# Kernel tuning notes

Hardware: AMD Instinct MI355X
Metric: run time of the kernel (lower is better)

## Reference

```python
import jax, jax.numpy as jnp
import numpy as np

D_MODEL = 1024
NUM_HEADS = 16
HEAD_DIM = D_MODEL // NUM_HEADS


def setup_inputs() -> dict:
    key = jax.random.key(0)
    ks = jax.random.split(key, 11)
    B, N = 2, 2048
    s = 1.0 / np.sqrt(D_MODEL)
    return {
        "query": jax.random.normal(ks[0], (B, N, D_MODEL), jnp.float32),
        "key":   jax.random.normal(ks[1], (B, N, D_MODEL), jnp.float32),
        "value": jax.random.normal(ks[2], (B, N, D_MODEL), jnp.float32),
        "Wq": jax.random.normal(ks[3], (D_MODEL, D_MODEL), jnp.float32) * s,
        "bq": jax.random.normal(ks[4], (D_MODEL,), jnp.float32) * 0.01,
        "Wk": jax.random.normal(ks[5], (D_MODEL, D_MODEL), jnp.float32) * s,
        "bk": jax.random.normal(ks[6], (D_MODEL,), jnp.float32) * 0.01,
        "Wv": jax.random.normal(ks[7], (D_MODEL, D_MODEL), jnp.float32) * s,
        "bv": jax.random.normal(ks[8], (D_MODEL,), jnp.float32) * 0.01,
        "Wo": jax.random.normal(ks[9], (D_MODEL, D_MODEL), jnp.float32) * s,
        "bo": jax.random.normal(ks[10], (D_MODEL,), jnp.float32) * 0.01,
    }


def _split_heads(x):
    # [B, N, d_model] -> [B, H, N, head_dim]
    B, N, _ = x.shape
    return x.reshape(B, N, NUM_HEADS, HEAD_DIM).transpose(0, 2, 1, 3)


def reference(query, key, value, Wq, bq, Wk, bk, Wv, bv, Wo, bo):
    B, N, _ = query.shape
    q = _split_heads(query @ Wq.T + bq)  # [B,H,N,dh]
    k = _split_heads(key @ Wk.T + bk)
    v = _split_heads(value @ Wv.T + bv)
    # NOTE: faithful to source: no 1/sqrt(head_dim) scaling.
    scores = jnp.einsum("bhnd,bhmd->bhnm", q, k)
    attn = jax.nn.softmax(scores, axis=-1)
    out = jnp.einsum("bhnm,bhmd->bhnd", attn, v)
    out = out.transpose(0, 2, 1, 3).reshape(B, N, D_MODEL)
    return out @ Wo.T + bo
```

## Files before the change

kernel.cpp:

```cpp
#include <hip/hip_runtime.h>
#include <cstdint>

#define DEV __device__ __forceinline__

typedef __bf16 bf16x8 __attribute__((ext_vector_type(8)));
typedef short s16x8 __attribute__((ext_vector_type(8)));
typedef float f32x4 __attribute__((ext_vector_type(4)));
typedef unsigned short u16;

constexpr int D_MODEL = 1024;
constexpr int SEQ = 2048;
constexpr float LOG2E = 1.4426950408889634f;
constexpr float SHIFT = 64.0f;

DEV u16 f2bf(float f) {
  uint32_t u = __float_as_uint(f);
  u += 0x7fff + ((u >> 16) & 1);
  return (u16)(u >> 16);
}

DEV void load_lds16(const void* g, void* l) {
  __builtin_amdgcn_global_load_lds((const __attribute__((address_space(1))) void*)g,
                                   (__attribute__((address_space(3))) void*)l, 16, 0, 0);
}

struct ConvArgs {
  const float* src[7];
  u16* dst[7];
  int n[7];
};

__global__ __launch_bounds__(256) void convert_kernel(ConvArgs a) {
  const int t = blockIdx.y;
  const int i = (blockIdx.x * 256 + threadIdx.x) * 4;
  if (i >= a.n[t]) return;
  const float4 v = *(const float4*)(a.src[t] + i);
  ushort4 o;
  o.x = f2bf(v.x); o.y = f2bf(v.y); o.z = f2bf(v.z); o.w = f2bf(v.w);
  *(ushort4*)(a.dst[t] + i) = o;
}

struct GemmArgs {
  const u16* A[3];
  const u16* W[3];
  const float* bias[3];
  void* out[3];
  float scale[3];
  int mode;
};

__global__ __launch_bounds__(256) void gemm_nt(GemmArgs args) {
  __shared__ u16 lA[128 * 64];
  __shared__ u16 lB[128 * 64];
  const int z = blockIdx.z;
  const u16* __restrict__ A = args.A[z];
  const u16* __restrict__ W = args.W[z];
  const int tid = threadIdx.x;
  const int lane = tid & 63, wid = tid >> 6;
  const int quad = lane >> 4, l16 = lane & 15;
  const int wm = wid >> 1, wn = wid & 1;
  const int m0 = blockIdx.y * 128;
  const int n0 = blockIdx.x * 128;

  f32x4 acc[4][4] = {};

  for (int kt = 0; kt < D_MODEL / 64; ++kt) {
    const int k0 = kt * 64;
#pragma unroll
    for (int p = 0; p < 4; ++p) {
      int c = p * 256 + tid;
      int row = c >> 3;
      int g = ((c & 7) ^ (row & 7)) * 8;
      load_lds16(A + (size_t)(m0 + row) * D_MODEL + k0 + g, &lA[c * 8]);
      load_lds16(W + (size_t)(n0 + row) * D_MODEL + k0 + g, &lB[c * 8]);
    }
    __syncthreads();
#pragma unroll
    for (int ks = 0; ks < 2; ++ks) {
      bf16x8 af[4], bfr[4];
#pragma unroll
      for (int mt = 0; mt < 4; ++mt) {
        int r = wm * 64 + mt * 16 + l16;
        int ch = (ks * 4 + quad) ^ (r & 7);
        af[mt] = *(const bf16x8*)&lA[r * 64 + ch * 8];
      }
#pragma unroll
      for (int nt = 0; nt < 4; ++nt) {
        int r = wn * 64 + nt * 16 + l16;
        int ch = (ks * 4 + quad) ^ (r & 7);
        bfr[nt] = *(const bf16x8*)&lB[r * 64 + ch * 8];
      }
#pragma unroll
      for (int mt = 0; mt < 4; ++mt)
#pragma unroll
        for (int nt = 0; nt < 4; ++nt)
          acc[mt][nt] = __builtin_amdgcn_mfma_f32_16x16x32_bf16(af[mt], bfr[nt], acc[mt][nt], 0, 0, 0);
    }
    __syncthreads();
  }

  const float* __restrict__ bias = args.bias[z];
  if (args.mode == 0) {
    u16* out = (u16*)args.out[z];
    float sc = args.scale[z];
#pragma unroll
    for (int nt = 0; nt < 4; ++nt) {
      int col = n0 + wn * 64 + nt * 16 + l16;
      float bv = bias[col];
      int h = col >> 6, d = col & 63;
#pragma unroll
      for (int mt = 0; mt < 4; ++mt) {
        int mb = m0 + wm * 64 + mt * 16 + quad * 4;
#pragma unroll
        for (int r = 0; r < 4; ++r) {
          int tok = mb + r;
          int b = tok >> 11, tt = tok & 2047;
          out[(((size_t)(b * 16 + h) * SEQ + tt) << 6) + d] = f2bf((acc[mt][nt][r] + bv) * sc);
        }
      }
    }
  } else {
    float* out = (float*)args.out[z];
#pragma unroll
    for (int nt = 0; nt < 4; ++nt) {
      int col = n0 + wn * 64 + nt * 16 + l16;
      float bv = bias[col];
#pragma unroll
      for (int mt = 0; mt < 4; ++mt) {
        int mb = m0 + wm * 64 + mt * 16 + quad * 4;
#pragma unroll
        for (int r = 0; r < 4; ++r)
          out[(size_t)(mb + r) * D_MODEL + col] = acc[mt][nt][r] + bv;
      }
    }
  }
}

__global__ __launch_bounds__(256) void transpose_v(const u16* __restrict__ V, u16* __restrict__ Vt) {
  __shared__ u16 tile[64][66];
  const int bh = blockIdx.y;
  const int t0 = blockIdx.x * 64;
  const int tid = threadIdx.x;
  const u16* src = V + ((size_t)bh * SEQ + t0) * 64;
#pragma unroll
  for (int p = 0; p < 4; ++p) {
    int v = p * 256 + tid;
    int row = v >> 4, c4 = (v & 15) * 4;
    ushort4 x = *(const ushort4*)(src + (size_t)row * 64 + c4);
    tile[row][c4] = x.x; tile[row][c4 + 1] = x.y; tile[row][c4 + 2] = x.z; tile[row][c4 + 3] = x.w;
  }
  __syncthreads();
  u16* dst = Vt + (size_t)bh * 64 * SEQ + t0;
#pragma unroll
  for (int p = 0; p < 4; ++p) {
    int v = p * 256 + tid;
    int d = v >> 4, c4 = (v & 15) * 4;
    ushort4 o;
    o.x = tile[c4][d]; o.y = tile[c4 + 1][d]; o.z = tile[c4 + 2][d]; o.w = tile[c4 + 3][d];
    *(ushort4*)(dst + (size_t)d * SEQ + c4) = o;
  }
}

__global__ __launch_bounds__(128, 2) void attn_kernel(const u16* __restrict__ Q,
                                                      const u16* __restrict__ K,
                                                      const u16* __restrict__ Vt,
                                                      u16* __restrict__ O) {
  __shared__ u16 sm[2][2][64 * 64];
  const int bid = blockIdx.x;
  const int xcd = bid & 7, jj = bid >> 3;
  const int bh = xcd + 8 * (jj >> 5);
  const int q0 = (jj & 31) * 64;
  const int tid = threadIdx.x;
  const int lane = tid & 63, w = tid >> 6;
  const int quad = lane >> 4, l16 = lane & 15;

  const u16* kbase = K + (size_t)bh * SEQ * 64;
  const u16* vtbase = Vt + (size_t)bh * 64 * SEQ;

  bf16x8 qf[4][2];
#pragma unroll
  for (int qh = 0; qh < 4; ++qh) {
    const u16* qrow = Q + ((size_t)bh * SEQ + q0 + qh * 16 + l16) * 64;
    qf[qh][0] = *(const bf16x8*)(qrow + quad * 8);
    qf[qh][1] = *(const bf16x8*)(qrow + 32 + quad * 8);
  }

  bf16x8 onesA;
  {
    __bf16 v = (l16 == 0) ? (__bf16)1.0f : (__bf16)0.0f;
#pragma unroll
    for (int j = 0; j < 8; ++j) onesA[j] = v;
  }

  f32x4 acc[4][5] = {};
  const f32x4 minit = {-SHIFT, -SHIFT, -SHIFT, -SHIFT};

#define STAGE(T, B)                                                               \
  {                                                                               \
    _Pragma("unroll")                                                             \
    for (int p = 0; p < 4; ++p) {                                                 \
      int c = p * 128 + tid;                                                      \
      int row = c >> 3;                                                           \
      int km = (row & 32) | (((row >> 2) & 3) << 3) | (((row >> 4) & 1) << 2) |   \
               (row & 3);                                                         \
      int g = ((c & 7) ^ (row & 7)) * 8;                                          \
      load_lds16(kbase + (size_t)((T) * 64 + km) * 64 + g, &sm[B][0][c * 8]);     \
      load_lds16(vtbase + (size_t)row * SEQ + (T) * 64 + g, &sm[B][1][c * 8]);    \
    }                                                                             \
  }

  STAGE(0, 0);
  __syncthreads();

  for (int t = 0; t < SEQ / 64; ++t) {
    if (t + 1 < SEQ / 64) STAGE(t + 1, (t + 1) & 1);
    const u16* lK = sm[t & 1][0];
    const u16* lV = sm[t & 1][1];

    bf16x8 kf[2][2];
#pragma unroll
    for (int nt = 0; nt < 2; ++nt) {
      int r = w * 32 + nt * 16 + l16;
#pragma unroll
      for (int ks = 0; ks < 2; ++ks) {
        int ch = (ks * 4 + quad) ^ (r & 7);
        kf[nt][ks] = *(const bf16x8*)&lK[r * 64 + ch * 8];
      }
    }

    s16x8 pf[4];
#pragma unroll
    for (int qh = 0; qh < 4; ++qh) {
      f32x4 s0 = __builtin_amdgcn_mfma_f32_16x16x32_bf16(kf[0][0], qf[qh][0], minit, 0, 0, 0);
      s0 = __builtin_amdgcn_mfma_f32_16x16x32_bf16(kf[0][1], qf[qh][1], s0, 0, 0, 0);
      f32x4 s1 = __builtin_amdgcn_mfma_f32_16x16x32_bf16(kf[1][0], qf[qh][0], minit, 0, 0, 0);
      s1 = __builtin_amdgcn_mfma_f32_16x16x32_bf16(kf[1][1], qf[qh][1], s1, 0, 0, 0);
      bf16x8 pb;
#pragma unroll
      for (int r = 0; r < 4; ++r) {
        pb[r] = (__bf16)__builtin_amdgcn_exp2f(s0[r]);
        pb[4 + r] = (__bf16)__builtin_amdgcn_exp2f(s1[r]);
      }
      pf[qh] = __builtin_bit_cast(s16x8, pb);
    }

#pragma unroll
    for (int dt = 0; dt < 4; ++dt) {
      int row = dt * 16 + l16;
      int ch = (w * 4 + quad) ^ (row & 7);
      bf16x8 vf = *(const bf16x8*)&lV[row * 64 + ch * 8];
#pragma unroll
      for (int qh = 0; qh < 4; ++qh)
        acc[qh][dt] = __builtin_amdgcn_mfma_f32_16x16x32_bf16(
            vf, __builtin_bit_cast(bf16x8, pf[qh]), acc[qh][dt], 0, 0, 0);
    }
#pragma unroll
    for (int qh = 0; qh < 4; ++qh)
      acc[qh][4] = __builtin_amdgcn_mfma_f32_16x16x32_bf16(
          onesA, __builtin_bit_cast(bf16x8, pf[qh]), acc[qh][4], 0, 0, 0);

    __syncthreads();
  }
#undef STAGE

  float* red = (float*)&sm[0][0][0];
  if (w == 1) {
#pragma unroll
    for (int qh = 0; qh < 4; ++qh)
#pragma unroll
      for (int dt = 0; dt < 5; ++dt)
        *(f32x4*)&red[((qh * 5 + dt) * 64 + lane) * 4] = acc[qh][dt];
  }
  __syncthreads();
  if (w == 0) {
    const int b = bh >> 4, h = bh & 15;
#pragma unroll
    for (int qh = 0; qh < 4; ++qh) {
#pragma unroll
      for (int dt = 0; dt < 5; ++dt)
        acc[qh][dt] += *(const f32x4*)&red[((qh * 5 + dt) * 64 + lane) * 4];
      float sum = __shfl(acc[qh][4][0], l16, 64);
      float inv = 1.0f / sum;
      const int tok = b * SEQ + q0 + qh * 16 + l16;
      u16* obase = O + (size_t)tok * D_MODEL + h * 64;
#pragma unroll
      for (int dt = 0; dt < 4; ++dt) {
        ushort4 o;
        o.x = f2bf(acc[qh][dt][0] * inv);
        o.y = f2bf(acc[qh][dt][1] * inv);
        o.z = f2bf(acc[qh][dt][2] * inv);
        o.w = f2bf(acc[qh][dt][3] * inv);
        *(ushort4*)(obase + dt * 16 + quad * 4) = o;
      }
    }
  }
}

extern "C" void kernel_launch(void* const* d_in, const int* in_sizes, int n_in,
                              void* d_out, int out_size, void* d_ws, size_t ws_size,
                              hipStream_t stream) {
  const float* q  = (const float*)d_in[0];
  const float* k  = (const float*)d_in[1];
  const float* v  = (const float*)d_in[2];
  const float* Wq = (const float*)d_in[3];
  const float* bq = (const float*)d_in[4];
  const float* Wk = (const float*)d_in[5];
  const float* bk = (const float*)d_in[6];
  const float* Wv = (const float*)d_in[7];
  const float* bv = (const float*)d_in[8];
  const float* Wo = (const float*)d_in[9];
  const float* bo = (const float*)d_in[10];

  uint8_t* ws = (uint8_t*)d_ws;
  const size_t MB = 1024 * 1024;
  u16* Xq  = (u16*)(ws + 0 * MB);
  u16* Xk  = (u16*)(ws + 8 * MB);
  u16* Xv  = (u16*)(ws + 16 * MB);
  u16* Wqb = (u16*)(ws + 24 * MB);
  u16* Wkb = (u16*)(ws + 26 * MB);
  u16* Wvb = (u16*)(ws + 28 * MB);
  u16* Wob = (u16*)(ws + 30 * MB);
  u16* Qb  = (u16*)(ws + 32 * MB);
  u16* Kb  = (u16*)(ws + 40 * MB);
  u16* Vb  = (u16*)(ws + 48 * MB);
  u16* Vtb = Xk;
  u16* Ob  = Xq;

  ConvArgs ca;
  ca.src[0] = q;  ca.dst[0] = Xq;  ca.n[0] = 4194304;
  ca.src[1] = k;  ca.dst[1] = Xk;  ca.n[1] = 4194304;
  ca.src[2] = v;  ca.dst[2] = Xv;  ca.n[2] = 4194304;
  ca.src[3] = Wq; ca.dst[3] = Wqb; ca.n[3] = 1048576;
  ca.src[4] = Wk; ca.dst[4] = Wkb; ca.n[4] = 1048576;
  ca.src[5] = Wv; ca.dst[5] = Wvb; ca.n[5] = 1048576;
  ca.src[6] = Wo; ca.dst[6] = Wob; ca.n[6] = 1048576;
  convert_kernel<<<dim3(4096, 7), 256, 0, stream>>>(ca);

  GemmArgs ga;
  ga.A[0] = Xq; ga.A[1] = Xk; ga.A[2] = Xv;
  ga.W[0] = Wqb; ga.W[1] = Wkb; ga.W[2] = Wvb;
  ga.bias[0] = bq; ga.bias[1] = bk; ga.bias[2] = bv;
  ga.out[0] = Qb; ga.out[1] = Kb; ga.out[2] = Vb;
  ga.scale[0] = LOG2E; ga.scale[1] = 1.0f; ga.scale[2] = 1.0f;
  ga.mode = 0;
  gemm_nt<<<dim3(8, 32, 3), 256, 0, stream>>>(ga);

  transpose_v<<<dim3(32, 32), 256, 0, stream>>>(Vb, Vtb);

  attn_kernel<<<dim3(1024), 128, 0, stream>>>(Qb, Kb, Vtb, Ob);

  GemmArgs g2;
  g2.A[0] = Ob; g2.A[1] = Ob; g2.A[2] = Ob;
  g2.W[0] = Wob; g2.W[1] = Wob; g2.W[2] = Wob;
  g2.bias[0] = bo; g2.bias[1] = bo; g2.bias[2] = bo;
  g2.out[0] = d_out; g2.out[1] = d_out; g2.out[2] = d_out;
  g2.scale[0] = 1.0f; g2.scale[1] = 1.0f; g2.scale[2] = 1.0f;
  g2.mode = 1;
  gemm_nt<<<dim3(8, 32, 1), 256, 0, stream>>>(g2);
}
```

Baseline: 231.2 us.

## Double-buffer GEMM LDS, XCD-aware block mapping, split-K output projection with atomics

The GEMM kernel now double-buffers its LDS tiles so the next K-slice loads while MFMAs run on the current one. Blocks are launched on a 1-D grid and remapped so that each XCD gets contiguous M rows, which should improve L2 reuse. The output projection is split four ways along K and accumulated with float atomicAdd into an output that the convert kernel first fills with the bias. This adds parallelism for the small final GEMM, at the cost of atomic traffic, doubled LDS use and a non-deterministic summation order.

Measured after the change: 256.2 us. +10.8%, slower.

```diff
diff --git a/kernel.cpp b/kernel.cpp
--- a/kernel.cpp
+++ b/kernel.cpp
@@ -25,15 +25,21 @@
 }
 
 struct ConvArgs {
-  const float* src[7];
+  const float* src[8];
   u16* dst[7];
-  int n[7];
+  float* dstf;
+  int n[8];
 };
 
 __global__ __launch_bounds__(256) void convert_kernel(ConvArgs a) {
   const int t = blockIdx.y;
   const int i = (blockIdx.x * 256 + threadIdx.x) * 4;
   if (i >= a.n[t]) return;
+  if (t == 7) {
+    float4 b = *(const float4*)(a.src[7] + (i & 1023));
+    *(float4*)(a.dstf + i) = b;
+    return;
+  }
   const float4 v = *(const float4*)(a.src[t] + i);
   ushort4 o;
   o.x = f2bf(v.x); o.y = f2bf(v.y); o.z = f2bf(v.z); o.w = f2bf(v.w);
@@ -46,35 +52,55 @@
   const float* bias[3];
   void* out[3];
   float scale[3];
-  int mode;
 };
 
-__global__ __launch_bounds__(256) void gemm_nt(GemmArgs args) {
-  __shared__ u16 lA[128 * 64];
-  __shared__ u16 lB[128 * 64];
-  const int z = blockIdx.z;
+template<int MODE>
+__global__ __launch_bounds__(256, 2) void gemm_nt(GemmArgs args) {
+  __shared__ u16 lds[2][2][128 * 64];
+  const int bid = blockIdx.x;
+  const int xcd = bid & 7, j = bid >> 3;
+  int z, m0, n0, kt0, ktN;
+  if (MODE == 0) {
+    z = j >> 5;
+    const int r = j & 31;
+    m0 = (xcd * 4 + (r >> 3)) * 128;
+    n0 = (r & 7) * 128;
+    kt0 = 0; ktN = 16;
+  } else {
+    z = 0;
+    const int mg = j >> 5, rest = j & 31;
+    m0 = (xcd * 4 + mg) * 128;
+    n0 = (rest >> 2) * 128;
+    kt0 = (rest & 3) * 4; ktN = kt0 + 4;
+  }
   const u16* __restrict__ A = args.A[z];
   const u16* __restrict__ W = args.W[z];
   const int tid = threadIdx.x;
   const int lane = tid & 63, wid = tid >> 6;
   const int quad = lane >> 4, l16 = lane & 15;
   const int wm = wid >> 1, wn = wid & 1;
-  const int m0 = blockIdx.y * 128;
-  const int n0 = blockIdx.x * 128;
 
   f32x4 acc[4][4] = {};
 
-  for (int kt = 0; kt < D_MODEL / 64; ++kt) {
-    const int k0 = kt * 64;
-#pragma unroll
-    for (int p = 0; p < 4; ++p) {
-      int c = p * 256 + tid;
-      int row = c >> 3;
-      int g = ((c & 7) ^ (row & 7)) * 8;
-      load_lds16(A + (size_t)(m0 + row) * D_MODEL + k0 + g, &lA[c * 8]);
-      load_lds16(W + (size_t)(n0 + row) * D_MODEL + k0 + g, &lB[c * 8]);
-    }
-    __syncthreads();
+#define GSTAGE(T, B)                                                              \
+  {                                                                               \
+    _Pragma("unroll")                                                             \
+    for (int p = 0; p < 4; ++p) {                                                 \
+      int c = p * 256 + tid;                                                      \
+      int row = c >> 3;                                                           \
+      int g = ((c & 7) ^ (row & 7)) * 8;                                          \
+      load_lds16(A + (size_t)(m0 + row) * D_MODEL + (T) * 64 + g, &lds[B][0][c * 8]); \
+      load_lds16(W + (size_t)(n0 + row) * D_MODEL + (T) * 64 + g, &lds[B][1][c * 8]); \
+    }                                                                             \
+  }
+
+  GSTAGE(kt0, 0);
+  __syncthreads();
+
+  for (int kt = kt0; kt < ktN; ++kt) {
+    if (kt + 1 < ktN) GSTAGE(kt + 1, (kt + 1) & 1);
+    const u16* lA = lds[kt & 1][0];
+    const u16* lB = lds[kt & 1][1];
 #pragma unroll
     for (int ks = 0; ks < 2; ++ks) {
       bf16x8 af[4], bfr[4];
@@ -98,9 +124,10 @@
     }
     __syncthreads();
   }
-
-  const float* __restrict__ bias = args.bias[z];
-  if (args.mode == 0) {
+#undef GSTAGE
+
+  if (MODE == 0) {
+    const float* __restrict__ bias = args.bias[z];
     u16* out = (u16*)args.out[z];
     float sc = args.scale[z];
 #pragma unroll
@@ -120,17 +147,16 @@
       }
     }
   } else {
-    float* out = (float*)args.out[z];
+    float* out = (float*)args.out[0];
 #pragma unroll
     for (int nt = 0; nt < 4; ++nt) {
       int col = n0 + wn * 64 + nt * 16 + l16;
-      float bv = bias[col];
 #pragma unroll
       for (int mt = 0; mt < 4; ++mt) {
         int mb = m0 + wm * 64 + mt * 16 + quad * 4;
 #pragma unroll
         for (int r = 0; r < 4; ++r)
-          out[(size_t)(mb + r) * D_MODEL + col] = acc[mt][nt][r] + bv;
+          atomicAdd(out + (size_t)(mb + r) * D_MODEL + col, acc[mt][nt][r]);
       }
     }
   }
@@ -334,7 +360,8 @@
   ca.src[4] = Wk; ca.dst[4] = Wkb; ca.n[4] = 1048576;
   ca.src[5] = Wv; ca.dst[5] = Wvb; ca.n[5] = 1048576;
   ca.src[6] = Wo; ca.dst[6] = Wob; ca.n[6] = 1048576;
-  convert_kernel<<<dim3(4096, 7), 256, 0, stream>>>(ca);
+  ca.src[7] = bo; ca.dstf = (float*)d_out; ca.n[7] = 4194304;
+  convert_kernel<<<dim3(4096, 8), 256, 0, stream>>>(ca);
 
   GemmArgs ga;
   ga.A[0] = Xq; ga.A[1] = Xk; ga.A[2] = Xv;
@@ -342,8 +369,7 @@
   ga.bias[0] = bq; ga.bias[1] = bk; ga.bias[2] = bv;
   ga.out[0] = Qb; ga.out[1] = Kb; ga.out[2] = Vb;
   ga.scale[0] = LOG2E; ga.scale[1] = 1.0f; ga.scale[2] = 1.0f;
-  ga.mode = 0;
-  gemm_nt<<<dim3(8, 32, 3), 256, 0, stream>>>(ga);
+  gemm_nt<0><<<dim3(768), 256, 0, stream>>>(ga);
 
   transpose_v<<<dim3(32, 32), 256, 0, stream>>>(Vb, Vtb);
 
@@ -355,6 +381,5 @@
   g2.bias[0] = bo; g2.bias[1] = bo; g2.bias[2] = bo;
   g2.out[0] = d_out; g2.out[1] = d_out; g2.out[2] = d_out;
   g2.scale[0] = 1.0f; g2.scale[1] = 1.0f; g2.scale[2] = 1.0f;
-  g2.mode = 1;
-  gemm_nt<<<dim3(8, 32, 1), 256, 0, stream>>>(g2);
-}
+  gemm_nt<1><<<dim3(1024), 256, 0, stream>>>(g2);
+}
```
